# Kernel optimization log

Measured on AMD Instinct MI355X. Metric: run time of the kernel, lower is better.

The kernel has to match this reference:

```python
import jax, jax.numpy as jnp
import numpy as np

D_MODEL = 2048
NUM_HEADS = 32
HEAD_DIM = D_MODEL // NUM_HEADS  # 64
ROPE_BASE = 10000.0


def _rope_cos_sin(seq_len, head_dim, dtype):
    inv_freq = 1.0 / (ROPE_BASE ** (jnp.arange(0, head_dim, 2, dtype=jnp.float32) / head_dim))
    freqs = jnp.arange(seq_len, dtype=jnp.float32)[:, None] * inv_freq[None, :]  # (S, Dh/2)
    emb = jnp.concatenate([freqs, freqs], axis=-1)  # (S, Dh)
    return emb.astype(dtype), jnp.cos(emb).astype(dtype), jnp.sin(emb).astype(dtype)


def _rotate_half(x):
    x1, x2 = jnp.split(x, 2, axis=-1)
    return jnp.concatenate([-x2, x1], axis=-1)


def setup_inputs() -> dict:
    key = jax.random.key(0)
    k1, k2, k3, k4 = jax.random.split(key, 4)
    B, S, D = 1, 2048, D_MODEL
    x = jax.random.normal(k1, (B, S, D), dtype=jnp.float32)
    Wqkv = jax.random.normal(k2, (3 * D, D), dtype=jnp.float32) * 0.02
    Wo = jax.random.normal(k3, (D, D), dtype=jnp.float32) * 0.02
    gate = jax.random.normal(k4, (D,), dtype=jnp.float32) * 0.1
    return {"x": x, "Wqkv": Wqkv, "Wo": Wo, "gate": gate}


def reference(x, Wqkv, Wo, gate):
    B, S, D = x.shape
    H, Dh = NUM_HEADS, HEAD_DIM
    residual = x

    # fused QKV projection (torch Linear: y = x @ W.T)
    qkv = jnp.einsum('bsd,ed->bse', x, Wqkv).reshape(B, S, 3, H, Dh)
    q, k, v = qkv[:, :, 0], qkv[:, :, 1], qkv[:, :, 2]  # each (B, S, H, Dh)

    # RoPE
    _, cos, sin = _rope_cos_sin(S, Dh, x.dtype)
    cos = cos[None, :, None, :]  # (1, S, 1, Dh)
    sin = sin[None, :, None, :]
    q = q * cos + _rotate_half(q) * sin
    k = k * cos + _rotate_half(k) * sin

    # causal SDPA
    scale = 1.0 / np.sqrt(Dh)
    scores = jnp.einsum('bqhd,bkhd->bhqk', q, k) * scale  # (B, H, S, S)
    causal = jnp.tril(jnp.ones((S, S), dtype=bool))
    scores = jnp.where(causal[None, None], scores, jnp.finfo(scores.dtype).min)
    probs = jax.nn.softmax(scores, axis=-1)
    attn = jnp.einsum('bhqk,bkhd->bqhd', probs, v).reshape(B, S, D)

    out = jnp.einsum('bsd,ed->bse', attn, Wo)
    # HeoGate: learned per-channel gated residual (assumption; see notes)
    return residual + gate * out
```

## Files before the change

kernel.cpp:

```cpp
#include <hip/hip_runtime.h>
#include <hip/hip_bf16.h>
#include <cstdint>
#include <cstddef>

typedef __hip_bfloat16 bf16;
typedef short short8 __attribute__((ext_vector_type(8)));
typedef float f32x4 __attribute__((ext_vector_type(4)));

#define S_LEN 2048
#define DMODEL 2048
#define NQKV 6144
#define NHEADS 32
#define HDIM 64
#define ROPE_L2 0.4152410118609203f

__device__ __forceinline__ void async_copy16(const bf16* g, bf16* l) {
  __builtin_amdgcn_global_load_lds(
      (const __attribute__((address_space(1))) void*)g,
      (__attribute__((address_space(3))) void*)l, 16, 0, 0);
}

__device__ __forceinline__ f32x4 mfma_bf16(short8 a, short8 b, f32x4 c) {
  return __builtin_amdgcn_mfma_f32_16x16x32_bf16(a, b, c, 0, 0, 0);
}

__global__ __launch_bounds__(256) void cvt3_kernel(const float* __restrict__ sx,
                                                   bf16* __restrict__ dx,
                                                   const float* __restrict__ sw,
                                                   bf16* __restrict__ dw,
                                                   const float* __restrict__ so,
                                                   bf16* __restrict__ dov) {
  int i = blockIdx.x * 256 + threadIdx.x;
  const float* s;
  bf16* d;
  if (i < 1048576) {
    s = sx; d = dx;
  } else if (i < 4194304) {
    s = sw; d = dw; i -= 1048576;
  } else {
    s = so; d = dov; i -= 4194304;
  }
  const float4 v = ((const float4*)s)[i];
  union { bf16 h[4]; ushort4 u; } tmp;
  tmp.h[0] = __float2bfloat16(v.x);
  tmp.h[1] = __float2bfloat16(v.y);
  tmp.h[2] = __float2bfloat16(v.z);
  tmp.h[3] = __float2bfloat16(v.w);
  ((ushort4*)d)[i] = tmp.u;
}

#define QKV_NT 32
#define QBAR() do { __builtin_amdgcn_s_barrier(); __builtin_amdgcn_sched_barrier(0); } while (0)
#define WAITV(n) asm volatile("s_waitcnt vmcnt(" #n ")" ::: "memory")
#define LGKM0() do { asm volatile("s_waitcnt lgkmcnt(0)" ::: "memory"); \
                     __builtin_amdgcn_sched_barrier(0); } while (0)

__global__ __launch_bounds__(512, 2) void gemm_qkv(const bf16* __restrict__ A,
                                                   const bf16* __restrict__ W,
                                                   bf16* __restrict__ q_ws,
                                                   bf16* __restrict__ k_ws,
                                                   bf16* __restrict__ v_ws) {
  __shared__ bf16 smem[65536];
  const int tid = threadIdx.x;
  const int wave = tid >> 6, lane = tid & 63;
  const int wm = wave >> 2, wn = wave & 3;
  const int m0 = blockIdx.y * 256, n0 = blockIdx.x * 256;
  const int swc = (((lane & 3) ^ ((lane >> 3) & 3)) * 8);
  const int fr = lane & 15, fq = lane >> 4;
  const int rdc = ((fq ^ ((fr >> 1) & 3)) * 8);
  const int srg = wave * 16 + (lane >> 2);

  auto stageA = [&](int t_, int kk_, int off_) {
#pragma unroll
    for (int rd = 0; rd < 2; ++rd)
      async_copy16(A + (size_t)(m0 + rd * 128 + srg) * DMODEL + t_ * 64 + kk_ * 32 + swc,
                   &smem[off_ + (rd * 128 + wave * 16) * 32]);
  };
  auto stageB = [&](int t_, int kk_, int off_) {
#pragma unroll
    for (int rd = 0; rd < 2; ++rd)
      async_copy16(W + (size_t)(n0 + rd * 128 + srg) * DMODEL + t_ * 64 + kk_ * 32 + swc,
                   &smem[off_ + (rd * 128 + wave * 16) * 32]);
  };

  const f32x4 zero = {0.f, 0.f, 0.f, 0.f};
  f32x4 acc[8][4];
#pragma unroll
  for (int i = 0; i < 8; ++i)
#pragma unroll
    for (int j = 0; j < 4; ++j) acc[i][j] = zero;
  short8 a[4], b[4];

  stageA(0, 0, 0);
  stageB(0, 0, 16384);
  stageA(0, 1, 8192);
  stageB(0, 1, 24576);
  stageA(1, 0, 32768);
  stageB(1, 0, 32768 + 16384);
  WAITV(8);
  QBAR();

#define LOAD_A(KK, MB, BC)                                                        \
  {                                                                               \
    const bf16* sA_ = &smem[(BC) * 32768 + (KK) * 8192];                          \
    _Pragma("unroll") for (int mi = 0; mi < 4; ++mi)                              \
        a[mi] = *(const short8*)&sA_[(wm * 128 + (MB) + mi * 16 + fr) * 32 + rdc];\
  }
#define LOAD_B(KK, BC)                                                            \
  {                                                                               \
    const bf16* sB_ = &smem[(BC) * 32768 + 16384 + (KK) * 8192];                  \
    _Pragma("unroll") for (int n = 0; n < 4; ++n)                                 \
        b[n] = *(const short8*)&sB_[(wn * 64 + n * 16 + fr) * 32 + rdc];          \
  }
#define MFMA16(MB)                                                                \
  __builtin_amdgcn_s_setprio(1);                                                  \
  _Pragma("unroll") for (int mi = 0; mi < 4; ++mi)                                \
      _Pragma("unroll") for (int n = 0; n < 4; ++n)                               \
          acc[(MB) / 16 + mi][n] = mfma_bf16(a[mi], b[n], acc[(MB) / 16 + mi][n]);\
  __builtin_amdgcn_s_setprio(0);

#pragma unroll 2
  for (int t = 0; t < QKV_NT; ++t) {
    const int bc = t & 1, bn = bc ^ 1;
    LOAD_A(0, 0, bc); LOAD_B(0, bc);
    if (t + 1 < QKV_NT) stageA(t + 1, 1, bn * 32768 + 8192);
    QBAR(); LGKM0();
    MFMA16(0);
    QBAR();
    LOAD_A(0, 64, bc);
    if (t + 1 < QKV_NT) stageB(t + 1, 1, bn * 32768 + 24576);
    QBAR(); LGKM0();
    MFMA16(64);
    if (t < QKV_NT - 1) { WAITV(8); } else { WAITV(0); }
    QBAR();
    LOAD_A(1, 64, bc); LOAD_B(1, bc);
    if (t + 2 < QKV_NT) stageA(t + 2, 0, bc * 32768);
    QBAR(); LGKM0();
    MFMA16(64);
    QBAR();
    LOAD_A(1, 0, bc);
    if (t + 2 < QKV_NT) stageB(t + 2, 0, bc * 32768 + 16384);
    QBAR(); LGKM0();
    MFMA16(0);
    if (t < QKV_NT - 2) { WAITV(8); }
    else if (t == QKV_NT - 2) { WAITV(4); }
    QBAR();
  }
#undef LOAD_A
#undef LOAD_B
#undef MFMA16

  const int colb = n0 + wn * 64;
  const int sect = colb >> 11;
  const int h = (colb & 2047) >> 6;
  const int col = fr, rq = fq * 4;

  if (sect < 2) {
    bf16* dst = ((sect == 0) ? q_ws : k_ws) + (size_t)h * S_LEN * HDIM;
    bf16* rep = smem + wave * 1152;
    const float f0 = exp2f(-(float)col * ROPE_L2);
    const float f1 = exp2f(-(float)(16 + col) * ROPE_L2);
    __syncthreads();
    for (int m = 0; m < 8; ++m) {
      const int base_s = m0 + wm * 128 + m * 16;
#pragma unroll
      for (int jl = 0; jl < 2; ++jl) {
        const int dh = jl * 16 + col;
        const float fr_ = (jl == 0) ? f0 : f1;
#pragma unroll
        for (int r = 0; r < 4; ++r) {
          const int srow = base_s + rq + r;
          float sn, cs;
          __sincosf((float)srow * fr_, &sn, &cs);
          const float xl = acc[m][jl][r], xh = acc[m][jl + 2][r];
          rep[(rq + r) * 72 + dh]      = __float2bfloat16(xl * cs - xh * sn);
          rep[(rq + r) * 72 + dh + 32] = __float2bfloat16(xh * cs + xl * sn);
        }
      }
#pragma unroll
      for (int p = 0; p < 2; ++p) {
        const int rr = p * 8 + (lane >> 3), ch = lane & 7;
        const uint4 vv = *(const uint4*)&rep[rr * 72 + ch * 8];
        *(uint4*)&dst[(size_t)(base_s + rr) * HDIM + ch * 8] = vv;
      }
    }
  } else {
    bf16* dst = v_ws + (size_t)h * HDIM * S_LEN;
    for (int j = 0; j < 4; ++j) {
      const int dh = j * 16 + col;
      for (int m = 0; m < 8; ++m) {
        const int s0 = m0 + wm * 128 + m * 16 + rq;
        union { bf16 hx[4]; uint2 u; } vk;
#pragma unroll
        for (int r = 0; r < 4; ++r) vk.hx[r] = __float2bfloat16(acc[m][j][r]);
        *(uint2*)&dst[(size_t)dh * S_LEN + s0] = vk.u;
      }
    }
  }
}

__global__ __launch_bounds__(512) void attn_kernel(const bf16* __restrict__ q_ws,
                                                   const bf16* __restrict__ k_ws,
                                                   const bf16* __restrict__ vt_ws,
                                                   bf16* __restrict__ attn_out) {
  const int bid = blockIdx.x;
  const int qt = 15 - (bid >> 5);
  const int h = bid & 31;

  const int tid = threadIdx.x, wave = tid >> 6, lane = tid & 63;
  const int col = lane & 15, fq = lane >> 4;
  const int q_glob = qt * 128 + wave * 16 + col;

  __shared__ bf16 Ks[2][64 * 64];
  __shared__ bf16 Vs[2][64 * 64];
  __shared__ bf16 Pl[8][16 * 72];
  bf16* pl = Pl[wave];

  const bf16* qh = q_ws + (size_t)h * S_LEN * HDIM;
  const bf16* kh = k_ws + (size_t)h * S_LEN * HDIM;
  const bf16* vh = vt_ws + (size_t)h * HDIM * S_LEN;

  const int srow = lane >> 3;
  const int slot = lane & 7;
  const int schunk = slot ^ srow;

  auto stage = [&](int kt, int buf) {
    const int k0 = kt * 64;
    const int r8 = wave * 8;
    async_copy16(kh + (size_t)(k0 + r8 + srow) * HDIM + schunk * 8,
                 &Ks[buf][r8 * 64]);
    async_copy16(vh + (size_t)(r8 + srow) * S_LEN + k0 + schunk * 8,
                 &Vs[buf][r8 * 64]);
  };

  short8 qf[2];
#pragma unroll
  for (int ks = 0; ks < 2; ++ks)
    qf[ks] = *(const short8*)&qh[(size_t)q_glob * HDIM + ks * 32 + fq * 8];

  const f32x4 zero = {0.f, 0.f, 0.f, 0.f};
  f32x4 o_acc[4] = {zero, zero, zero, zero};
  float m_i = -1e30f, l_i = 0.f;

  stage(0, 0);

  const int lastk = 2 * qt + 1;
  for (int kt = 0; kt <= lastk; ++kt) {
    const int buf = kt & 1;
    const int k0 = kt * 64;
    __syncthreads();
    if (kt < lastk) stage(kt + 1, buf ^ 1);

    short8 kf[8];
#pragma unroll
    for (int n = 0; n < 4; ++n) {
      const int row = n * 16 + col;
#pragma unroll
      for (int ks = 0; ks < 2; ++ks)
        kf[n * 2 + ks] =
            *(const short8*)&Ks[buf][row * 64 + (((ks * 4 + fq) ^ (row & 7)) * 8)];
    }
    f32x4 s_acc[4] = {zero, zero, zero, zero};
#pragma unroll
    for (int n = 0; n < 4; ++n)
#pragma unroll
      for (int ks = 0; ks < 2; ++ks)
        s_acc[n] = mfma_bf16(kf[n * 2 + ks], qf[ks], s_acc[n]);

    short8 vf[8];
#pragma unroll
    for (int n = 0; n < 4; ++n) {
      const int row = n * 16 + col;
#pragma unroll
      for (int ks = 0; ks < 2; ++ks)
        vf[n * 2 + ks] =
            *(const short8*)&Vs[buf][row * 64 + (((ks * 4 + fq) ^ (row & 7)) * 8)];
    }

    if (k0 + 63 > qt * 128 + wave * 16) {
#pragma unroll
      for (int n = 0; n < 4; ++n)
#pragma unroll
        for (int r = 0; r < 4; ++r)
          if (k0 + n * 16 + fq * 4 + r > q_glob) s_acc[n][r] = -1e30f;
    }

    float vmax = -1e30f;
#pragma unroll
    for (int n = 0; n < 4; ++n)
#pragma unroll
      for (int r = 0; r < 4; ++r) vmax = fmaxf(vmax, s_acc[n][r]);
    vmax = fmaxf(vmax, __shfl_xor(vmax, 16, 64));
    vmax = fmaxf(vmax, __shfl_xor(vmax, 32, 64));

    if (!__all(vmax - m_i <= 8.0f)) {
      const float mnew = fmaxf(m_i, vmax);
      const float alpha = __expf((m_i - mnew) * 0.125f);
      l_i *= alpha;
#pragma unroll
      for (int n = 0; n < 4; ++n)
#pragma unroll
        for (int r = 0; r < 4; ++r) o_acc[n][r] *= alpha;
      m_i = mnew;
    }

    float rs = 0.f;
#pragma unroll
    for (int n = 0; n < 4; ++n)
#pragma unroll
      for (int r = 0; r < 4; ++r) {
        const float p = __expf((s_acc[n][r] - m_i) * 0.125f);
        s_acc[n][r] = p;
        rs += p;
      }
    rs += __shfl_xor(rs, 16, 64);
    rs += __shfl_xor(rs, 32, 64);
    l_i += rs;

#pragma unroll
    for (int n = 0; n < 4; ++n) {
      union { bf16 hx[4]; uint2 u; } pk;
#pragma unroll
      for (int r = 0; r < 4; ++r) pk.hx[r] = __float2bfloat16(s_acc[n][r]);
      *(uint2*)&pl[col * 72 + n * 16 + fq * 4] = pk.u;
    }
    short8 pa[2];
#pragma unroll
    for (int ks = 0; ks < 2; ++ks)
      pa[ks] = *(const short8*)&pl[col * 72 + ks * 32 + fq * 8];

#pragma unroll
    for (int n = 0; n < 4; ++n)
#pragma unroll
      for (int ks = 0; ks < 2; ++ks)
        o_acc[n] = mfma_bf16(vf[n * 2 + ks], pa[ks], o_acc[n]);
  }

  const float inv = 1.0f / l_i;
#pragma unroll
  for (int n = 0; n < 4; ++n) {
#pragma unroll
    for (int r = 0; r < 4; ++r) o_acc[n][r] *= inv;
    union { bf16 hx[4]; uint2 u; } ok;
#pragma unroll
    for (int r = 0; r < 4; ++r) ok.hx[r] = __float2bfloat16(o_acc[n][r]);
    *(uint2*)&attn_out[(size_t)q_glob * DMODEL + h * HDIM + n * 16 + fq * 4] = ok.u;
  }
}

__global__ __launch_bounds__(256) void gemm_out(const bf16* __restrict__ A,
                                                const bf16* __restrict__ W,
                                                const float* __restrict__ xres,
                                                const float* __restrict__ gate,
                                                float* __restrict__ out) {
  constexpr int K = DMODEL;
  constexpr int NT = K / 32;
  __shared__ bf16 As[3][64 * 32];
  __shared__ bf16 Bs[3][128 * 32];
  const int tid = threadIdx.x;
  const int wave = tid >> 6, lane = tid & 63;
  const int m0 = blockIdx.y * 64, n0 = blockIdx.x * 128;
  const int sr = lane >> 2;
  const int swc = (((lane & 3) ^ ((lane >> 3) & 3)) * 8);
  const int fr = lane & 15, fq = lane >> 4;
  const int rdc = ((fq ^ ((fr >> 1) & 3)) * 8);

  auto stage = [&](int t_, int s_) {
    async_copy16(A + (size_t)(m0 + wave * 16 + sr) * K + t_ * 32 + swc,
                 &As[s_][(wave * 16) * 32]);
#pragma unroll
    for (int j = 0; j < 2; ++j)
      async_copy16(W + (size_t)(n0 + wave * 32 + j * 16 + sr) * K + t_ * 32 + swc,
                   &Bs[s_][(wave * 32 + j * 16) * 32]);
  };

  const f32x4 zero = {0.f, 0.f, 0.f, 0.f};
  f32x4 acc[4][2];
  for (int i = 0; i < 4; ++i)
    for (int j = 0; j < 2; ++j) acc[i][j] = zero;

  stage(0, 0);
  stage(1, 1);
  WAITV(3);
  QBAR();

  for (int t = 0; t < NT; ++t) {
    const int s = t % 3;
    short8 a[4], b[2];
#pragma unroll
    for (int i = 0; i < 4; ++i)
      a[i] = *(const short8*)&As[s][(i * 16 + fr) * 32 + rdc];
#pragma unroll
    for (int j = 0; j < 2; ++j)
      b[j] = *(const short8*)&Bs[s][(wave * 32 + j * 16 + fr) * 32 + rdc];
    LGKM0();
    QBAR();
    if (t + 2 < NT) stage(t + 2, (t + 2) % 3);
#pragma unroll
    for (int i = 0; i < 4; ++i)
#pragma unroll
      for (int j = 0; j < 2; ++j)
        acc[i][j] = mfma_bf16(a[i], b[j], acc[i][j]);
    if (t + 1 < NT) {
      if (t + 2 < NT) { WAITV(3); }
      else            { WAITV(0); }
      QBAR();
    }
  }

  const int col = fr, rq = fq * 4;
  for (int j = 0; j < 2; ++j) {
    const int cc = n0 + wave * 32 + j * 16 + col;
    const float g = gate[cc];
    for (int i = 0; i < 4; ++i) {
      const int base_row = m0 + i * 16 + rq;
      for (int r = 0; r < 4; ++r) {
        const size_t idx = (size_t)(base_row + r) * DMODEL + cc;
        out[idx] = xres[idx] + g * acc[i][j][r];
      }
    }
  }
}

extern "C" void kernel_launch(void* const* d_in, const int* in_sizes, int n_in,
                              void* d_out, int out_size, void* d_ws, size_t ws_size,
                              hipStream_t stream) {
  const float* x    = (const float*)d_in[0];
  const float* Wqkv = (const float*)d_in[1];
  const float* Wo   = (const float*)d_in[2];
  const float* gate = (const float*)d_in[3];
  float* out = (float*)d_out;

  char* ws = (char*)d_ws;
  const size_t MB = 1024 * 1024;
  bf16* xb      = (bf16*)(ws);
  bf16* wqkvb   = (bf16*)(ws + 8 * MB);
  bf16* wob     = (bf16*)(ws + 32 * MB);
  bf16* q_ws    = (bf16*)(ws + 40 * MB);
  bf16* k_ws    = (bf16*)(ws + 48 * MB);
  bf16* v_ws    = (bf16*)(ws + 56 * MB);
  bf16* attn_ws = (bf16*)(ws);

  cvt3_kernel<<<dim3(20480), 256, 0, stream>>>(x, xb, Wqkv, wqkvb, Wo, wob);

  gemm_qkv<<<dim3(NQKV / 256, S_LEN / 256), 512, 0, stream>>>(xb, wqkvb, q_ws, k_ws, v_ws);
  attn_kernel<<<dim3(512), 512, 0, stream>>>(q_ws, k_ws, v_ws, attn_ws);
  gemm_out<<<dim3(DMODEL / 128, DMODEL / 64), 256, 0, stream>>>(attn_ws, wob, x, gate, out);
}
```

Before: 251.9 us.

## Shrink QKV GEMM tiles to 128x128 with simpler double-buffered pipeline

Reduces the QKV projection block tile from 256x256 to 128x128, halving LDS use and raising the occupancy hint so four blocks can share a CU. The grid grows from 192 to 768 blocks, so all CUs are filled instead of leaving many idle. The K-loop is simplified to a two-stage double buffer with one async copy per thread per operand. In exchange, operand reuse per block drops and global/L2 traffic per FLOP rises.

Result: no change. 252.0 us (+0.1%).

```diff
diff --git a/kernel.cpp b/kernel.cpp
--- a/kernel.cpp
+++ b/kernel.cpp
@@ -55,100 +55,79 @@
 #define LGKM0() do { asm volatile("s_waitcnt lgkmcnt(0)" ::: "memory"); \
                      __builtin_amdgcn_sched_barrier(0); } while (0)
 
-__global__ __launch_bounds__(512, 2) void gemm_qkv(const bf16* __restrict__ A,
+__global__ __launch_bounds__(512, 4) void gemm_qkv(const bf16* __restrict__ A,
                                                    const bf16* __restrict__ W,
                                                    bf16* __restrict__ q_ws,
                                                    bf16* __restrict__ k_ws,
                                                    bf16* __restrict__ v_ws) {
-  __shared__ bf16 smem[65536];
+  __shared__ bf16 smem[32768];
   const int tid = threadIdx.x;
   const int wave = tid >> 6, lane = tid & 63;
-  const int wm = wave >> 2, wn = wave & 3;
-  const int m0 = blockIdx.y * 256, n0 = blockIdx.x * 256;
-  const int swc = (((lane & 3) ^ ((lane >> 3) & 3)) * 8);
+  const int wm = wave >> 1, wn = wave & 1;
+  const int m0 = blockIdx.y * 128, n0 = blockIdx.x * 128;
+  const int srow_g = tid >> 2;
+  const int swc = (((tid & 3) ^ ((tid >> 3) & 3)) * 8);
   const int fr = lane & 15, fq = lane >> 4;
   const int rdc = ((fq ^ ((fr >> 1) & 3)) * 8);
-  const int srg = wave * 16 + (lane >> 2);
-
-  auto stageA = [&](int t_, int kk_, int off_) {
-#pragma unroll
-    for (int rd = 0; rd < 2; ++rd)
-      async_copy16(A + (size_t)(m0 + rd * 128 + srg) * DMODEL + t_ * 64 + kk_ * 32 + swc,
-                   &smem[off_ + (rd * 128 + wave * 16) * 32]);
+
+  auto stageA = [&](int t_, int kk_, int bufe_) {
+    async_copy16(A + (size_t)(m0 + srow_g) * DMODEL + t_ * 64 + kk_ * 32 + swc,
+                 &smem[bufe_ + kk_ * 4096 + wave * 512]);
   };
-  auto stageB = [&](int t_, int kk_, int off_) {
-#pragma unroll
-    for (int rd = 0; rd < 2; ++rd)
-      async_copy16(W + (size_t)(n0 + rd * 128 + srg) * DMODEL + t_ * 64 + kk_ * 32 + swc,
-                   &smem[off_ + (rd * 128 + wave * 16) * 32]);
+  auto stageB = [&](int t_, int kk_, int bufe_) {
+    async_copy16(W + (size_t)(n0 + srow_g) * DMODEL + t_ * 64 + kk_ * 32 + swc,
+                 &smem[bufe_ + 8192 + kk_ * 4096 + wave * 512]);
   };
 
   const f32x4 zero = {0.f, 0.f, 0.f, 0.f};
-  f32x4 acc[8][4];
-#pragma unroll
-  for (int i = 0; i < 8; ++i)
+  f32x4 acc[2][4];
+#pragma unroll
+  for (int i = 0; i < 2; ++i)
 #pragma unroll
     for (int j = 0; j < 4; ++j) acc[i][j] = zero;
-  short8 a[4], b[4];
+  short8 a[2], b[4];
 
   stageA(0, 0, 0);
-  stageB(0, 0, 16384);
-  stageA(0, 1, 8192);
-  stageB(0, 1, 24576);
-  stageA(1, 0, 32768);
-  stageB(1, 0, 32768 + 16384);
-  WAITV(8);
+  stageB(0, 0, 0);
+  stageA(0, 1, 0);
+  stageB(0, 1, 0);
+  WAITV(2);
   QBAR();
 
-#define LOAD_A(KK, MB, BC)                                                        \
-  {                                                                               \
-    const bf16* sA_ = &smem[(BC) * 32768 + (KK) * 8192];                          \
-    _Pragma("unroll") for (int mi = 0; mi < 4; ++mi)                              \
-        a[mi] = *(const short8*)&sA_[(wm * 128 + (MB) + mi * 16 + fr) * 32 + rdc];\
-  }
+#define LOAD_A(KK, BC)                                                            \
+  _Pragma("unroll") for (int mi = 0; mi < 2; ++mi)                                \
+      a[mi] = *(const short8*)&smem[(BC) + (KK) * 4096 +                          \
+                                    (wm * 32 + mi * 16 + fr) * 32 + rdc];
 #define LOAD_B(KK, BC)                                                            \
-  {                                                                               \
-    const bf16* sB_ = &smem[(BC) * 32768 + 16384 + (KK) * 8192];                  \
-    _Pragma("unroll") for (int n = 0; n < 4; ++n)                                 \
-        b[n] = *(const short8*)&sB_[(wn * 64 + n * 16 + fr) * 32 + rdc];          \
-  }
-#define MFMA16(MB)                                                                \
+  _Pragma("unroll") for (int n = 0; n < 4; ++n)                                   \
+      b[n] = *(const short8*)&smem[(BC) + 8192 + (KK) * 4096 +                    \
+                                   (wn * 64 + n * 16 + fr) * 32 + rdc];
+#define MFMA8()                                                                   \
   __builtin_amdgcn_s_setprio(1);                                                  \
-  _Pragma("unroll") for (int mi = 0; mi < 4; ++mi)                                \
+  _Pragma("unroll") for (int mi = 0; mi < 2; ++mi)                                \
       _Pragma("unroll") for (int n = 0; n < 4; ++n)                               \
-          acc[(MB) / 16 + mi][n] = mfma_bf16(a[mi], b[n], acc[(MB) / 16 + mi][n]);\
+          acc[mi][n] = mfma_bf16(a[mi], b[n], acc[mi][n]);                        \
   __builtin_amdgcn_s_setprio(0);
 
 #pragma unroll 2
   for (int t = 0; t < QKV_NT; ++t) {
-    const int bc = t & 1, bn = bc ^ 1;
-    LOAD_A(0, 0, bc); LOAD_B(0, bc);
-    if (t + 1 < QKV_NT) stageA(t + 1, 1, bn * 32768 + 8192);
+    const int bc = (t & 1) * 16384, bn = ((t + 1) & 1) * 16384;
+    LOAD_A(0, bc); LOAD_B(0, bc);
+    if (t + 1 < QKV_NT) { stageA(t + 1, 0, bn); stageB(t + 1, 0, bn); }
     QBAR(); LGKM0();
-    MFMA16(0);
+    MFMA8();
+    if (t + 1 < QKV_NT) { WAITV(2); } else { WAITV(0); }
     QBAR();
-    LOAD_A(0, 64, bc);
-    if (t + 1 < QKV_NT) stageB(t + 1, 1, bn * 32768 + 24576);
+    LOAD_A(1, bc); LOAD_B(1, bc);
+    if (t + 1 < QKV_NT) { stageA(t + 1, 1, bn); stageB(t + 1, 1, bn); }
     QBAR(); LGKM0();
-    MFMA16(64);
-    if (t < QKV_NT - 1) { WAITV(8); } else { WAITV(0); }
-    QBAR();
-    LOAD_A(1, 64, bc); LOAD_B(1, bc);
-    if (t + 2 < QKV_NT) stageA(t + 2, 0, bc * 32768);
-    QBAR(); LGKM0();
-    MFMA16(64);
-    QBAR();
-    LOAD_A(1, 0, bc);
-    if (t + 2 < QKV_NT) stageB(t + 2, 0, bc * 32768 + 16384);
-    QBAR(); LGKM0();
-    MFMA16(0);
-    if (t < QKV_NT - 2) { WAITV(8); }
-    else if (t == QKV_NT - 2) { WAITV(4); }
+    MFMA8();
+    if (t + 1 < QKV_NT) { WAITV(2); }
     QBAR();
   }
 #undef LOAD_A
 #undef LOAD_B
-#undef MFMA16
+#undef MFMA8
 
   const int colb = n0 + wn * 64;
   const int sect = colb >> 11;
@@ -161,8 +140,8 @@
     const float f0 = exp2f(-(float)col * ROPE_L2);
     const float f1 = exp2f(-(float)(16 + col) * ROPE_L2);
     __syncthreads();
-    for (int m = 0; m < 8; ++m) {
-      const int base_s = m0 + wm * 128 + m * 16;
+    for (int m = 0; m < 2; ++m) {
+      const int base_s = m0 + wm * 32 + m * 16;
 #pragma unroll
       for (int jl = 0; jl < 2; ++jl) {
         const int dh = jl * 16 + col;
@@ -188,8 +167,8 @@
     bf16* dst = v_ws + (size_t)h * HDIM * S_LEN;
     for (int j = 0; j < 4; ++j) {
       const int dh = j * 16 + col;
-      for (int m = 0; m < 8; ++m) {
-        const int s0 = m0 + wm * 128 + m * 16 + rq;
+      for (int m = 0; m < 2; ++m) {
+        const int s0 = m0 + wm * 32 + m * 16 + rq;
         union { bf16 hx[4]; uint2 u; } vk;
 #pragma unroll
         for (int r = 0; r < 4; ++r) vk.hx[r] = __float2bfloat16(acc[m][j][r]);
@@ -443,7 +422,7 @@
 
   cvt3_kernel<<<dim3(20480), 256, 0, stream>>>(x, xb, Wqkv, wqkvb, Wo, wob);
 
-  gemm_qkv<<<dim3(NQKV / 256, S_LEN / 256), 512, 0, stream>>>(xb, wqkvb, q_ws, k_ws, v_ws);
+  gemm_qkv<<<dim3(NQKV / 128, S_LEN / 128), 512, 0, stream>>>(xb, wqkvb, q_ws, k_ws, v_ws);
   attn_kernel<<<dim3(512), 512, 0, stream>>>(q_ws, k_ws, v_ws, attn_ws);
   gemm_out<<<dim3(DMODEL / 128, DMODEL / 64), 256, 0, stream>>>(attn_ws, wob, x, gate, out);
 }
```
